# Performance work log

Hardware: AMD Instinct MI355X
Metric: run time of the kernel (lower is better)

Reference implementation:

```python
import jax, jax.numpy as jnp
import numpy as np
from jax import lax

ALPHA = 0.6
BETA = 0.4
GROUP = 22   # players per match (fixed group size)
TOPK = 11    # dream11 team size; min(11, 22) == 11
M = 500_000  # number of match groups
N = M * GROUP


def setup_inputs() -> dict:
    key = jax.random.key(0)
    k1, k2 = jax.random.split(key)
    pred = jax.random.normal(k1, (N,), dtype=jnp.float32)
    target = jax.random.normal(k2, (N,), dtype=jnp.float32)
    # contiguous equal-size groups: [0,0,...,0, 1,1,...,1, ...]
    batch_ids = jnp.repeat(jnp.arange(M, dtype=jnp.int64), GROUP)
    return {"pred": pred, "target": target, "batch_ids": batch_ids}


def _overlap_penalty(p, t):
    # p, t: [M, GROUP]
    m = p.shape[0]
    _, pi = lax.top_k(p, TOPK)  # [M, TOPK] indices within group
    _, ti = lax.top_k(t, TOPK)
    rows = jnp.arange(m)[:, None]
    pm = jnp.zeros((m, GROUP), dtype=bool).at[rows, pi].set(True)
    tm = jnp.zeros((m, GROUP), dtype=bool).at[rows, ti].set(True)
    overlap = jnp.sum(pm & tm, axis=-1)  # [M] set-intersection size
    penalty = 1.0 - overlap.astype(p.dtype) / TOPK
    return jnp.mean(penalty)


def reference(pred, target, batch_ids):
    mse = jnp.mean((pred - target) ** 2)
    # batch_ids are sorted contiguous equal-size groups of GROUP rows
    m = pred.shape[0] // GROUP
    p = pred.reshape(m, GROUP)
    t = target.reshape(m, GROUP)
    overlap_loss = _overlap_penalty(p, t)
    return ALPHA * mse + BETA * overlap_loss
```

## Files before the change

kernel.cpp:

```cpp
#include <hip/hip_runtime.h>

#define ALPHA_C 0.6f
#define BETA_C  0.4f
#define GROUP_C 22
#define TOPK_C  11
#define BLOCK_C 256

__global__ __launch_bounds__(BLOCK_C, 4) void ol_main(
    const float* __restrict__ pred, const float* __restrict__ target,
    int M, float* __restrict__ ws_s, float* __restrict__ ws_o)
{
    int g = blockIdx.x * BLOCK_C + threadIdx.x;
    float s = 0.0f;
    int ov = 0;

    if (g < M) {
        float p[GROUP_C], t[GROUP_C];
        const float2* gp = (const float2*)(pred + (size_t)g * GROUP_C);
        const float2* gt = (const float2*)(target + (size_t)g * GROUP_C);
#pragma unroll
        for (int j = 0; j < GROUP_C / 2; ++j) {
            float2 v = gp[j]; p[2 * j] = v.x; p[2 * j + 1] = v.y;
            float2 w = gt[j]; t[2 * j] = w.x; t[2 * j + 1] = w.y;
        }

#pragma unroll
        for (int j = 0; j < GROUP_C; ++j) {
            float d = p[j] - t[j];
            s = fmaf(d, d, s);
        }

#pragma unroll
        for (int j = 0; j < GROUP_C; ++j) {
            float pj = p[j], tj = t[j];
            int cp = 0, ct = 0;
#pragma unroll
            for (int k = 0; k < GROUP_C; ++k) {
                if (k < j) {
                    cp += (p[k] >= pj) ? 1 : 0;
                    ct += (t[k] >= tj) ? 1 : 0;
                } else if (k > j) {
                    cp += (p[k] > pj) ? 1 : 0;
                    ct += (t[k] > tj) ? 1 : 0;
                }
            }
            ov += (cp < TOPK_C && ct < TOPK_C) ? 1 : 0;
        }
    }

    float fov = (float)ov;
#pragma unroll
    for (int off = 32; off > 0; off >>= 1) {
        s   += __shfl_down(s, off);
        fov += __shfl_down(fov, off);
    }

    __shared__ float sm_s[BLOCK_C / 64];
    __shared__ float sm_o[BLOCK_C / 64];
    int lane = threadIdx.x & 63;
    int wid  = threadIdx.x >> 6;
    if (lane == 0) { sm_s[wid] = s; sm_o[wid] = fov; }
    __syncthreads();

    if (threadIdx.x == 0) {
        float ss = sm_s[0] + sm_s[1] + sm_s[2] + sm_s[3];
        float oo = sm_o[0] + sm_o[1] + sm_o[2] + sm_o[3];
        ws_s[blockIdx.x] = ss;
        ws_o[blockIdx.x] = oo;
    }
}

__global__ __launch_bounds__(BLOCK_C) void ol_finalize(
    const float* __restrict__ ws_s, const float* __restrict__ ws_o,
    int nblocks, float* __restrict__ out, int M)
{
    float s = 0.0f, o = 0.0f;
    for (int i = threadIdx.x; i < nblocks; i += BLOCK_C) {
        s += ws_s[i];
        o += ws_o[i];
    }
#pragma unroll
    for (int off = 32; off > 0; off >>= 1) {
        s += __shfl_down(s, off);
        o += __shfl_down(o, off);
    }
    __shared__ float sm_s[BLOCK_C / 64];
    __shared__ float sm_o[BLOCK_C / 64];
    int lane = threadIdx.x & 63;
    int wid  = threadIdx.x >> 6;
    if (lane == 0) { sm_s[wid] = s; sm_o[wid] = o; }
    __syncthreads();
    if (threadIdx.x == 0) {
        float ss = sm_s[0] + sm_s[1] + sm_s[2] + sm_s[3];
        float oo = sm_o[0] + sm_o[1] + sm_o[2] + sm_o[3];
        float n   = (float)M * (float)GROUP_C;
        float mse = ss / n;
        float pen = 1.0f - oo / ((float)TOPK_C * (float)M);
        out[0] = ALPHA_C * mse + BETA_C * pen;
    }
}

extern "C" void kernel_launch(void* const* d_in, const int* in_sizes, int n_in,
                              void* d_out, int out_size, void* d_ws, size_t ws_size,
                              hipStream_t stream) {
    const float* pred   = (const float*)d_in[0];
    const float* target = (const float*)d_in[1];

    int N = in_sizes[0];
    int M = N / GROUP_C;
    int blocks = (M + BLOCK_C - 1) / BLOCK_C;

    float* ws_s = (float*)d_ws;
    float* ws_o = ws_s + blocks;

    hipLaunchKernelGGL(ol_main, dim3(blocks), dim3(BLOCK_C), 0, stream,
                       pred, target, M, ws_s, ws_o);
    hipLaunchKernelGGL(ol_finalize, dim3(1), dim3(BLOCK_C), 0, stream,
                       ws_s, ws_o, blocks, (float*)d_out, M);
}
```

Before: 156.6 us.

## Replace pairwise rank counting with bitonic-sort threshold selection for top-11

Instead of counting, for each of the 22 elements, how many others beat it (about 2x22x21 comparisons per group), each row is split into 16+6 elements. Both parts are sorted with compile-time bitonic networks of min/max ops, and a merge-style max-of-mins yields the 11th-largest value as a threshold. Membership is then a single comparison against that threshold. This cuts per-thread ALU work sharply. It changes tie semantics: with duplicate values at the threshold, more than 11 elements can count as selected, which differs from top_k's index-order tie-breaking.

Measured after the change: 142.8 us. -8.8%, faster.

```diff
diff --git a/kernel.cpp b/kernel.cpp
--- a/kernel.cpp
+++ b/kernel.cpp
@@ -5,6 +5,68 @@
 #define GROUP_C 22
 #define TOPK_C  11
 #define BLOCK_C 256
+#define NEG_BIG (-3.0e38f)
+
+
+__device__ __forceinline__ void ce_desc(float& x, float& y) {
+    float hi = fmaxf(x, y);
+    float lo = fminf(x, y);
+    x = hi; y = lo;
+}
+
+template<int I, int END, int R, int M>
+struct MLoop {
+    static __device__ __forceinline__ void run(float* a) {
+        if constexpr (I + R < END) {
+            ce_desc(a[I], a[I + R]);
+            MLoop<I + M, END, R, M>::run(a);
+        }
+    }
+};
+
+template<int LO, int N, int R>
+struct Merge {
+    static __device__ __forceinline__ void run(float* a) {
+        constexpr int M = R * 2;
+        if constexpr (M < N) {
+            Merge<LO, N, M>::run(a);
+            Merge<LO + R, N, M>::run(a);
+            MLoop<LO + R, LO + N, R, M>::run(a);
+        } else {
+            ce_desc(a[LO], a[LO + R]);
+        }
+    }
+};
+
+template<int LO, int N>
+struct Sort {
+    static __device__ __forceinline__ void run(float* a) {
+        if constexpr (N > 1) {
+            Sort<LO, N / 2>::run(a);
+            Sort<LO + N / 2, N / 2>::run(a);
+            Merge<LO, N, 1>::run(a);
+        }
+    }
+};
+
+__device__ __forceinline__ float sel11_of_22(const float* v) {
+    float A[16], B[8];
+#pragma unroll
+    for (int i = 0; i < 16; ++i) A[i] = v[i];
+#pragma unroll
+    for (int i = 0; i < 6; ++i) B[i] = v[16 + i];
+    B[6] = NEG_BIG; B[7] = NEG_BIG;
+    Sort<0, 16>::run(A);
+    Sort<0, 8>::run(B);
+    float thr = A[10];
+    thr = fmaxf(thr, fminf(A[9], B[0]));
+    thr = fmaxf(thr, fminf(A[8], B[1]));
+    thr = fmaxf(thr, fminf(A[7], B[2]));
+    thr = fmaxf(thr, fminf(A[6], B[3]));
+    thr = fmaxf(thr, fminf(A[5], B[4]));
+    thr = fmaxf(thr, fminf(A[4], B[5]));
+    return thr;
+}
 
 __global__ __launch_bounds__(BLOCK_C, 4) void ol_main(
     const float* __restrict__ pred, const float* __restrict__ target,
@@ -24,27 +86,14 @@
             float2 w = gt[j]; t[2 * j] = w.x; t[2 * j + 1] = w.y;
         }
 
+        float thr_p = sel11_of_22(p);
+        float thr_t = sel11_of_22(t);
+
 #pragma unroll
         for (int j = 0; j < GROUP_C; ++j) {
             float d = p[j] - t[j];
             s = fmaf(d, d, s);
-        }
-
-#pragma unroll
-        for (int j = 0; j < GROUP_C; ++j) {
-            float pj = p[j], tj = t[j];
-            int cp = 0, ct = 0;
-#pragma unroll
-            for (int k = 0; k < GROUP_C; ++k) {
-                if (k < j) {
-                    cp += (p[k] >= pj) ? 1 : 0;
-                    ct += (t[k] >= tj) ? 1 : 0;
-                } else if (k > j) {
-                    cp += (p[k] > pj) ? 1 : 0;
-                    ct += (t[k] > tj) ? 1 : 0;
-                }
-            }
-            ov += (cp < TOPK_C && ct < TOPK_C) ? 1 : 0;
+            ov += (p[j] >= thr_p && t[j] >= thr_t) ? 1 : 0;
         }
     }
 
```
